# Kernel optimization log

Hardware: AMD Instinct MI355X
Metric: run time of the kernel (lower is better)

Reference implementation:

```python
import jax, jax.numpy as jnp
import numpy as np

WEIGHT_ENERGY = 0.1
WEIGHT_COV = 0.005
EPS = 1e-9
COV_EPS = 1e-6
TWO_PI = 2.0 * np.pi


def setup_inputs() -> dict:
    key = jax.random.key(0)
    k1, k2 = jax.random.split(key)
    z = jax.random.normal(k1, (16, 256, 64, 32), dtype=jnp.float32)
    gamma = jax.random.uniform(k2, (16, 256, 64, 8), dtype=jnp.float32)
    return {"z": z, "gamma": gamma}


def _gmm_loss(z, gamma):
    # z: [B,T,F,D], gamma: [B,T,F,K]
    D = z.shape[-1]
    N = z.shape[0] * z.shape[1] * z.shape[2]
    sum_gamma = jnp.sum(gamma, axis=(0, 1, 2))            # [K]
    phi = sum_gamma / N                                    # [K]
    mu = jnp.einsum('btfk,btfd->kd', gamma, z) / sum_gamma[:, None]  # [K,D]
    z_mu = z[..., None, :] - mu                            # [B,T,F,K,D]
    # covariance per component (gamma-weighted outer products)
    cov = jnp.einsum('btfk,btfkd,btfke->kde', gamma, z_mu, z_mu) / sum_gamma[:, None, None]
    eye = jnp.eye(D, dtype=z.dtype)
    cov = cov + CO_EPS_I(eye)
    cov_k = cov + EPS * eye                                # [K,D,D]
    cov_inv = jnp.linalg.inv(cov_k)                        # [K,D,D]
    L = jnp.linalg.cholesky(cov_k * TWO_PI)                # [K,D,D]
    det_cov = jnp.prod(jnp.diagonal(L, axis1=-2, axis2=-1), axis=-1)  # [K] (= sqrt(det(2pi*cov)))
    cov_diag = jnp.sum(1.0 / jnp.diagonal(cov_k, axis1=-2, axis2=-1))
    # quadratic-form energy, fused reduction over D
    E_z = -0.5 * jnp.einsum('btfkd,kde,btfke->btfk', z_mu, cov_inv, z_mu)
    E_z = jnp.exp(E_z)
    E_z = -jnp.log(jnp.sum(phi * E_z / jnp.sqrt(det_cov), axis=-1) + COV_EPS)
    sample_energy = jnp.mean(E_z)
    sample_energy = jnp.where(jnp.isfinite(sample_energy), sample_energy, 0.0)
    cov_diag = jnp.where(jnp.isfinite(cov_diag), cov_diag, 0.0)
    return WEIGHT_ENERGY * sample_energy + WEIGHT_COV * cov_diag


def CO_EPS_I(eye):
    return COV_EPS * eye


def reference(z, gamma):
    return _gmm_loss(z, gamma)
```

## Files before the change

kernel.cpp:

```cpp
#include <hip/hip_runtime.h>
#include <hip/hip_bf16.h>
#include <math.h>

#define NS (16*256*64)
#define NCHUNK (NS/64)
#define D 32
#define K 8

typedef __attribute__((ext_vector_type(8))) short bf16x8;
typedef __attribute__((ext_vector_type(8))) float f32x8;
typedef __attribute__((ext_vector_type(8))) __bf16 bf16v8;
typedef __attribute__((ext_vector_type(16))) float f32x16;

#define WS_ENERGY   0
#define WS_COVDIAG  1
#define WS_DONE     2
#define WS_C        16
#define WS_COEF     24
#define WS_SG       32
#define WS_S1       64
#define WS_S2       1024
#define WS_FRAGA    9216
#define WS_FRAGB    13312
#define WS_PART     16384
#define PART_STRIDE 8456

__device__ __forceinline__ bf16x8 cvt8(f32x8 v) {
    union { bf16v8 h; bf16x8 s; } u;
    u.h = __builtin_convertvector(v, bf16v8);
    return u.s;
}
__device__ __forceinline__ unsigned short f2bf1(float f) {
    union { __bf16 h; unsigned short s; } u;
    u.h = (__bf16)f;
    return u.s;
}
__device__ __forceinline__ float bf2f(unsigned short u) {
    union { unsigned u32; float f; } v;
    v.u32 = ((unsigned)u) << 16;
    return v.f;
}
__device__ __forceinline__ float rdlane(float v, int lane) {
    return __uint_as_float(__builtin_amdgcn_readlane(__float_as_uint(v), lane));
}

__global__ __launch_bounds__(256) void k_moments(const float* __restrict__ z,
                                                 const float* __restrict__ g,
                                                 float* __restrict__ part) {
    __shared__ __align__(16) unsigned short zbt[32][72];
    __shared__ __align__(16) unsigned short gbt[8][72];
    const int t   = threadIdx.x;
    const int w   = t >> 6;
    const int l   = t & 63;
    const int col = l & 31;
    const int nh  = l >> 5;
    const int k0  = 2 * w;
    const int sz  = t >> 2;
    const int dq  = (t & 3) * 8;

    f32x16 acc0 = {}, acc1 = {};
    float s1a = 0.f, s1b = 0.f, sga = 0.f, sgb = 0.f;

    int c = blockIdx.x;
    float4 za, zb4, ga4, gb4;
    {
        const float* zp = z + ((size_t)(c * 64 + sz)) * 32 + dq;
        za  = *(const float4*)zp;
        zb4 = *(const float4*)(zp + 4);
        if (t < 64) {
            const float* gp = g + ((size_t)(c * 64 + t)) * 8;
            ga4 = *(const float4*)gp;
            gb4 = *(const float4*)(gp + 4);
        }
    }

    for (; c < NCHUNK; c += gridDim.x) {
        __syncthreads();
        {
            float zf8[8] = {za.x, za.y, za.z, za.w, zb4.x, zb4.y, zb4.z, zb4.w};
#pragma unroll
            for (int i = 0; i < 8; i++) {
                int d = dq + i;
                zbt[d][sz ^ (((d >> 3) & 3) << 3)] = f2bf1(zf8[i]);
            }
            if (t < 64) {
                float gf8[8] = {ga4.x, ga4.y, ga4.z, ga4.w, gb4.x, gb4.y, gb4.z, gb4.w};
#pragma unroll
                for (int k = 0; k < 8; k++) gbt[k][t] = f2bf1(gf8[k]);
            }
        }
        {
            int cn = c + gridDim.x;
            if (cn < NCHUNK) {
                const float* zp = z + ((size_t)(cn * 64 + sz)) * 32 + dq;
                za  = *(const float4*)zp;
                zb4 = *(const float4*)(zp + 4);
                if (t < 64) {
                    const float* gp = g + ((size_t)(cn * 64 + t)) * 8;
                    ga4 = *(const float4*)gp;
                    gb4 = *(const float4*)(gp + 4);
                }
            }
        }
        __syncthreads();
        const int xs = ((col >> 3) & 3) << 3;
#pragma unroll
        for (int sc = 0; sc < 4; sc++) {
            const int s0 = sc * 16 + nh * 8;
            bf16x8 af = *(const bf16x8*)&zbt[col][s0 ^ xs];
            bf16x8 g0 = *(const bf16x8*)&gbt[k0][s0];
            bf16x8 g1 = *(const bf16x8*)&gbt[k0 + 1][s0];
            f32x8 p0, p1;
#pragma unroll
            for (int j = 0; j < 8; j++) {
                float zf = bf2f((unsigned short)af[j]);
                float ga = bf2f((unsigned short)g0[j]);
                float gb = bf2f((unsigned short)g1[j]);
                p0[j] = ga * zf;
                p1[j] = gb * zf;
                s1a += p0[j];  s1b += p1[j];
                sga += ga;     sgb += gb;
            }
            acc0 = __builtin_amdgcn_mfma_f32_32x32x16_bf16(af, cvt8(p0), acc0, 0, 0, 0);
            acc1 = __builtin_amdgcn_mfma_f32_32x32x16_bf16(af, cvt8(p1), acc1, 0, 0, 0);
        }
    }
    s1a += __shfl_xor(s1a, 32);  s1b += __shfl_xor(s1b, 32);
    sga += __shfl_xor(sga, 32);  sgb += __shfl_xor(sgb, 32);

    float* pb = part + (size_t)blockIdx.x * PART_STRIDE;
#pragma unroll
    for (int r = 0; r < 16; r++) {
        int row = (r & 3) + 8 * (r >> 2) + 4 * nh;
        pb[(size_t)k0 * 1024 + row * 32 + col]       = acc0[r];
        pb[(size_t)(k0 + 1) * 1024 + row * 32 + col] = acc1[r];
    }
    if (l < 32) {
        pb[8192 + k0 * 32 + col]       = s1a;
        pb[8192 + (k0 + 1) * 32 + col] = s1b;
    }
    if (l == 0) { pb[8448 + k0] = sga; pb[8448 + k0 + 1] = sgb; }
}

__global__ __launch_bounds__(1024) void k_reduce(float* __restrict__ ws, int nblk) {
    __shared__ float red[16][64];
    const int t  = threadIdx.x;
    const int el = t & 63;
    const int bg = t >> 6;
    const int e  = blockIdx.x * 64 + el;
    const float* part = ws + WS_PART;
    float s = 0.0f;
    if (e < PART_STRIDE) {
        for (int b = bg; b < nblk; b += 16)
            s += part[(size_t)b * PART_STRIDE + e];
    }
    red[bg][el] = s;
    __syncthreads();
#pragma unroll
    for (int h = 8; h > 0; h >>= 1) {
        if (bg < h) red[bg][el] += red[bg + h][el];
        __syncthreads();
    }
    if (bg == 0 && e < PART_STRIDE) {
        float v = red[0][el];
        if (e < 8192)       ws[WS_S2 + e] = v;
        else if (e < 8448)  ws[WS_S1 + (e - 8192)] = v;
        else                ws[WS_SG + (e - 8448)] = v;
    }
    if (blockIdx.x == 0) {
        if (t < 512) ws[WS_FRAGB + t] = 0.0f;
        if (t == 0) {
            ws[WS_ENERGY] = 0.0f;
            ws[WS_COVDIAG] = 0.0f;
            ((unsigned*)ws)[WS_DONE] = 0u;
        }
    }
}

__global__ __launch_bounds__(64) void k_prep(float* __restrict__ ws) {
    __shared__ float Am[32][33];
    __shared__ float mus[32];
    __shared__ float bLs[32];

    const int k   = blockIdx.x;
    const int l   = threadIdx.x;
    const int c32 = l & 31;
    const bool right = l >= 32;

    const float sgk = ws[WS_SG + k];
    if (l < 32) mus[l] = ws[WS_S1 + k * 32 + l] / sgk;
    __syncthreads();
    const float mc  = mus[c32];
    const float rsg = 1.0f / sgk;

    float x[32];
    float dval = 1.0f;
#pragma unroll
    for (int r = 0; r < 32; r++) {
        float v;
        if (right) {
            v = (r == c32) ? 1.0f : 0.0f;
        } else {
            v = ws[WS_S2 + k * 1024 + r * 32 + c32] * rsg - mus[r] * mc;
            if (r == c32) { v += 1.0e-6f + 1.0e-9f; dval = v; }
        }
        x[r] = v;
    }

    {
        float tdi = right ? 0.0f : 1.0f / dval;
#pragma unroll
        for (int m = 1; m < 64; m <<= 1) tdi += __shfl_xor(tdi, m);
        if (l == 0) atomicAdd(&ws[WS_COVDIAG], tdi);
    }

    float logdet = 0.0f;
#pragma unroll
    for (int j = 0; j < 32; j++) {
        float piv = rdlane(x[j], j);
        float rp  = 1.0f / piv;
        logdet += __logf(piv);
        x[j] *= rp;
#pragma unroll
        for (int r = 0; r < 32; r++) {
            if (r == j) continue;
            float m = rdlane(x[r], j);
            x[r] -= m * x[j];
        }
    }
    if (right) {
#pragma unroll
        for (int r = 0; r < 32; r++) Am[r][c32] = x[r];
    }
    __syncthreads();

    if (l == 0) {
        float phi = sgk / (float)NS;
        ws[WS_COEF + k] = phi * __expf(-(8.0f * 1.8378770664093453f + 0.25f * logdet));
    }

    if (l < 32) {
        float s = 0.0f;
#pragma unroll
        for (int c = 0; c < 32; c++) s += Am[c32][c] * mus[c];
        bLs[c32] = s;
    }
    __syncthreads();
    {
        float cm = (l < 32) ? mus[c32] * bLs[c32] : 0.0f;
#pragma unroll
        for (int m = 1; m < 64; m <<= 1) cm += __shfl_xor(cm, m);
        if (l == 0) ws[WS_C + k] = cm;
    }

    {
        const int ph = l >> 5;
#pragma unroll
        for (int h = 0; h < 2; h++) {
            int r = c32, cb = ph * 8 + 16 * h;
            unsigned uu[4];
#pragma unroll
            for (int q = 0; q < 4; q++) {
                unsigned lo2 = f2bf1(Am[r][cb + 2 * q]);
                unsigned hi2 = f2bf1(Am[r][cb + 2 * q + 1]);
                uu[q] = lo2 | (hi2 << 16);
            }
            ((uint4*)(ws + WS_FRAGA))[(k * 2 + h) * 64 + l] = make_uint4(uu[0], uu[1], uu[2], uu[3]);
        }
        if (c32 == k) {
#pragma unroll
            for (int h = 0; h < 2; h++) {
                int cb = ph * 8 + 16 * h;
                unsigned uu[4];
#pragma unroll
                for (int q = 0; q < 4; q++) {
                    unsigned lo2 = f2bf1(bLs[cb + 2 * q]);
                    unsigned hi2 = f2bf1(bLs[cb + 2 * q + 1]);
                    uu[q] = lo2 | (hi2 << 16);
                }
                ((uint4*)(ws + WS_FRAGB))[h * 64 + l] = make_uint4(uu[0], uu[1], uu[2], uu[3]);
            }
        }
    }
}

__global__ __launch_bounds__(512) void k_energy(const float* __restrict__ z,
                                                float* __restrict__ ws,
                                                float* __restrict__ out) {
    __shared__ float redw[8];
    const int t   = threadIdx.x;
    const int w   = t >> 6;
    const int l   = t & 63;
    const int col = l & 31;
    const int nh  = l >> 5;

    const uint4* fragA = (const uint4*)(ws + WS_FRAGA);
    const uint4* fragB = (const uint4*)(ws + WS_FRAGB);
    float cf[8], cc[8];
#pragma unroll
    for (int k = 0; k < 8; k++) { cf[k] = ws[WS_COEF + k]; cc[k] = ws[WS_C + k]; }
    uint4 fbu0 = fragB[l];
    uint4 fbu1 = fragB[64 + l];

    float En = 0.0f;
    for (int ci = 0; ci < 2; ci++) {
        const int chunk = (blockIdx.x * 8 + w) * 2 + ci;
        const int n0 = chunk * 32;
        const float* zb = z + (size_t)(n0 + col) * 32 + nh * 8;
        float4 a0 = *(const float4*)(zb + 0);
        float4 a1 = *(const float4*)(zb + 4);
        float4 a2 = *(const float4*)(zb + 16);
        float4 a3 = *(const float4*)(zb + 20);
        f32x8 zlo = {a0.x,a0.y,a0.z,a0.w,a1.x,a1.y,a1.z,a1.w};
        f32x8 zhi = {a2.x,a2.y,a2.z,a2.w,a3.x,a3.y,a3.z,a3.w};
        bf16x8 b0 = cvt8(zlo), b1 = cvt8(zhi);
        float olo[4], ohi[4];
#pragma unroll
        for (int j = 0; j < 4; j++) {
            float mlo = nh ? zlo[j] : zlo[j + 4];
            float mhi = nh ? zhi[j] : zhi[j + 4];
            olo[j] = __shfl_xor(mlo, 32);
            ohi[j] = __shfl_xor(mhi, 32);
        }
        float zdot[16];
#pragma unroll
        for (int j = 0; j < 4; j++) {
            zdot[j]      = nh ? olo[j]     : zlo[j];
            zdot[4 + j]  = nh ? zlo[4 + j] : olo[j];
            zdot[8 + j]  = nh ? ohi[j]     : zhi[j];
            zdot[12 + j] = nh ? zhi[4 + j] : ohi[j];
        }
        f32x16 acc2 = {};
        acc2 = __builtin_amdgcn_mfma_f32_32x32x16_bf16(*(const bf16x8*)&fbu0, b0, acc2, 0, 0, 0);
        acc2 = __builtin_amdgcn_mfma_f32_32x32x16_bf16(*(const bf16x8*)&fbu1, b1, acc2, 0, 0, 0);
        float oth[4];
#pragma unroll
        for (int r = 0; r < 4; r++) oth[r] = __shfl_xor(acc2[r], 32);
        float pk[8];
#pragma unroll
        for (int k = 0; k < 8; k++) {
            uint4 fa0u = fragA[(k * 2 + 0) * 64 + l];
            uint4 fa1u = fragA[(k * 2 + 1) * 64 + l];
            f32x16 acc = {};
            acc = __builtin_amdgcn_mfma_f32_32x32x16_bf16(*(const bf16x8*)&fa0u, b0, acc, 0, 0, 0);
            acc = __builtin_amdgcn_mfma_f32_32x32x16_bf16(*(const bf16x8*)&fa1u, b1, acc, 0, 0, 0);
            float p = 0.0f;
#pragma unroll
            for (int r = 0; r < 16; r++) p += acc[r] * zdot[r];
            p += __shfl_xor(p, 32);
            pk[k] = p;
        }
        float ssum = 0.0f;
#pragma unroll
        for (int k = 0; k < 8; k++) {
            float d2 = (k < 4) ? (nh ? oth[k] : acc2[k]) : (nh ? acc2[k - 4] : oth[k - 4]);
            float E = pk[k] - 2.0f * d2 + cc[k];
            ssum += cf[k] * __expf(-0.5f * E);
        }
        En += -__logf(ssum + 1.0e-6f);
    }
#pragma unroll
    for (int m = 1; m < 64; m <<= 1) En += __shfl_xor(En, m);
    if (l == 0) redw[w] = En;
    __syncthreads();
    if (t == 0) {
        float s = 0.0f;
#pragma unroll
        for (int i = 0; i < 8; i++) s += redw[i];
        atomicAdd(&ws[WS_ENERGY], s);
        __threadfence();
        unsigned old = atomicAdd((unsigned*)ws + WS_DONE, 1u);
        if (old == gridDim.x - 1) {
            float se = atomicAdd(&ws[WS_ENERGY], 0.0f);
            se = se * 0.5f / (float)NS;
            if (!isfinite(se)) se = 0.0f;
            float cd = ws[WS_COVDIAG];
            if (!isfinite(cd)) cd = 0.0f;
            out[0] = 0.1f * se + 0.005f * cd;
        }
    }
}

extern "C" void kernel_launch(void* const* d_in, const int* in_sizes, int n_in,
                              void* d_out, int out_size, void* d_ws, size_t ws_size,
                              hipStream_t stream) {
    const float* z = (const float*)d_in[0];
    const float* g = (const float*)d_in[1];
    float* out = (float*)d_out;
    float* ws  = (float*)d_ws;

    long avail = (long)(ws_size / 4) - WS_PART;
    int nblk = (int)(avail / PART_STRIDE);
    if (nblk > 512) nblk = 512;
    if (nblk < 1)   nblk = 1;

    k_moments<<<nblk, 256, 0, stream>>>(z, g, ws + WS_PART);
    k_reduce<<<(PART_STRIDE + 63) / 64, 1024, 0, stream>>>(ws, nblk);
    k_prep<<<8, 64, 0, stream>>>(ws);
    k_energy<<<512, 512, 0, stream>>>(z, ws, out);
}
```

Before: 79.48 us.

## Fuse partial reduction and covariance prep into one last-block kernel

Merges the partial-sum reduction and the per-component covariance inversion into one kernel. The last block to finish, detected with an atomic counter, inverts all 8 covariances, one wavefront per component. Workspace scalars are now zeroed at the start of the moments kernel, and the gamma sums move out of the MFMA inner loop into the load stage, summed in fp32 and reduced once per block. This removes one kernel launch and some per-iteration ALU work. The trade-off is a serialized tail in a single block, and the explicit zeroing of the B-fragment buffer is dropped.

```diff
diff --git a/kernel.cpp b/kernel.cpp
--- a/kernel.cpp
+++ b/kernel.cpp
@@ -15,6 +15,7 @@
 #define WS_ENERGY   0
 #define WS_COVDIAG  1
 #define WS_DONE     2
+#define WS_DONE2    3
 #define WS_C        16
 #define WS_COEF     24
 #define WS_SG       32
@@ -46,10 +47,11 @@
 
 __global__ __launch_bounds__(256) void k_moments(const float* __restrict__ z,
                                                  const float* __restrict__ g,
-                                                 float* __restrict__ part) {
+                                                 float* __restrict__ ws) {
     __shared__ __align__(16) unsigned short zbt[32][72];
     __shared__ __align__(16) unsigned short gbt[8][72];
     const int t   = threadIdx.x;
+    const int bid = blockIdx.x;
     const int w   = t >> 6;
     const int l   = t & 63;
     const int col = l & 31;
@@ -58,10 +60,15 @@
     const int sz  = t >> 2;
     const int dq  = (t & 3) * 8;
 
+    if (bid == 0 && t < 64) ws[t] = 0.0f;
+
     f32x16 acc0 = {}, acc1 = {};
-    float s1a = 0.f, s1b = 0.f, sga = 0.f, sgb = 0.f;
-
-    int c = blockIdx.x;
+    float s1a = 0.f, s1b = 0.f;
+    float sg8[8];
+#pragma unroll
+    for (int k = 0; k < 8; k++) sg8[k] = 0.0f;
+
+    int c = bid;
     float4 za, zb4, ga4, gb4;
     {
         const float* zp = z + ((size_t)(c * 64 + sz)) * 32 + dq;
@@ -73,7 +80,6 @@
             gb4 = *(const float4*)(gp + 4);
         }
     }
-
     for (; c < NCHUNK; c += gridDim.x) {
         __syncthreads();
         {
@@ -86,7 +92,10 @@
             if (t < 64) {
                 float gf8[8] = {ga4.x, ga4.y, ga4.z, ga4.w, gb4.x, gb4.y, gb4.z, gb4.w};
 #pragma unroll
-                for (int k = 0; k < 8; k++) gbt[k][t] = f2bf1(gf8[k]);
+                for (int k = 0; k < 8; k++) {
+                    gbt[k][t] = f2bf1(gf8[k]);
+                    sg8[k] += gf8[k];
+                }
             }
         }
         {
@@ -114,21 +123,17 @@
 #pragma unroll
             for (int j = 0; j < 8; j++) {
                 float zf = bf2f((unsigned short)af[j]);
-                float ga = bf2f((unsigned short)g0[j]);
-                float gb = bf2f((unsigned short)g1[j]);
-                p0[j] = ga * zf;
-                p1[j] = gb * zf;
+                p0[j] = bf2f((unsigned short)g0[j]) * zf;
+                p1[j] = bf2f((unsigned short)g1[j]) * zf;
                 s1a += p0[j];  s1b += p1[j];
-                sga += ga;     sgb += gb;
             }
             acc0 = __builtin_amdgcn_mfma_f32_32x32x16_bf16(af, cvt8(p0), acc0, 0, 0, 0);
             acc1 = __builtin_amdgcn_mfma_f32_32x32x16_bf16(af, cvt8(p1), acc1, 0, 0, 0);
         }
     }
     s1a += __shfl_xor(s1a, 32);  s1b += __shfl_xor(s1b, 32);
-    sga += __shfl_xor(sga, 32);  sgb += __shfl_xor(sgb, 32);
-
-    float* pb = part + (size_t)blockIdx.x * PART_STRIDE;
+
+    float* pb = ws + WS_PART + (size_t)bid * PART_STRIDE;
 #pragma unroll
     for (int r = 0; r < 16; r++) {
         int row = (r & 3) + 8 * (r >> 2) + 4 * nh;
@@ -139,11 +144,24 @@
         pb[8192 + k0 * 32 + col]       = s1a;
         pb[8192 + (k0 + 1) * 32 + col] = s1b;
     }
-    if (l == 0) { pb[8448 + k0] = sga; pb[8448 + k0 + 1] = sgb; }
-}
-
-__global__ __launch_bounds__(1024) void k_reduce(float* __restrict__ ws, int nblk) {
+    if (t < 64) {
+#pragma unroll
+        for (int k = 0; k < 8; k++) {
+            float v = sg8[k];
+#pragma unroll
+            for (int m = 1; m < 64; m <<= 1) v += __shfl_xor(v, m);
+            if (t == 0) pb[8448 + k] = v;
+        }
+    }
+}
+
+__global__ __launch_bounds__(1024) void k_redprep(float* __restrict__ ws, int nblk) {
     __shared__ float red[16][64];
+    __shared__ float Am8[8][32][33];
+    __shared__ float mus8[8][32];
+    __shared__ float bLs8[8][32];
+    __shared__ unsigned lastflag;
+
     const int t  = threadIdx.x;
     const int el = t & 63;
     const int bg = t >> 6;
@@ -167,115 +185,107 @@
         else if (e < 8448)  ws[WS_S1 + (e - 8192)] = v;
         else                ws[WS_SG + (e - 8448)] = v;
     }
-    if (blockIdx.x == 0) {
-        if (t < 512) ws[WS_FRAGB + t] = 0.0f;
-        if (t == 0) {
-            ws[WS_ENERGY] = 0.0f;
-            ws[WS_COVDIAG] = 0.0f;
-            ((unsigned*)ws)[WS_DONE] = 0u;
-        }
-    }
-}
-
-__global__ __launch_bounds__(64) void k_prep(float* __restrict__ ws) {
-    __shared__ float Am[32][33];
-    __shared__ float mus[32];
-    __shared__ float bLs[32];
-
-    const int k   = blockIdx.x;
-    const int l   = threadIdx.x;
+    __syncthreads();
+    if (t == 0) {
+        __threadfence();
+        unsigned old = atomicAdd((unsigned*)ws + WS_DONE2, 1u);
+        lastflag = (old == gridDim.x - 1) ? 1u : 0u;
+    }
+    __syncthreads();
+    if (!lastflag) return;
+
+    const int w8  = t >> 6;
+    const int l   = t & 63;
     const int c32 = l & 31;
-    const bool right = l >= 32;
-
-    const float sgk = ws[WS_SG + k];
-    if (l < 32) mus[l] = ws[WS_S1 + k * 32 + l] / sgk;
-    __syncthreads();
-    const float mc  = mus[c32];
-    const float rsg = 1.0f / sgk;
-
-    float x[32];
-    float dval = 1.0f;
-#pragma unroll
-    for (int r = 0; r < 32; r++) {
-        float v;
+    const bool pa    = (w8 < 8);
+    const bool right = pa && (l >= 32);
+
+    float sgk = 1.0f;
+    if (pa) sgk = ws[WS_SG + w8];
+    if (pa && l < 32) mus8[w8][l] = ws[WS_S1 + w8 * 32 + l] / sgk;
+    __syncthreads();
+
+    float logdet = 0.0f;
+    if (pa) {
+        const float mc  = mus8[w8][c32];
+        const float rsg = 1.0f / sgk;
+        float x[32];
+        float dval = 1.0f;
+#pragma unroll
+        for (int r = 0; r < 32; r++) {
+            float v;
+            if (right) {
+                v = (r == c32) ? 1.0f : 0.0f;
+            } else {
+                v = ws[WS_S2 + w8 * 1024 + r * 32 + c32] * rsg - mus8[w8][r] * mc;
+                if (r == c32) { v += 1.0e-6f + 1.0e-9f; dval = v; }
+            }
+            x[r] = v;
+        }
+        {
+            float tdi = right ? 0.0f : 1.0f / dval;
+#pragma unroll
+            for (int m = 1; m < 64; m <<= 1) tdi += __shfl_xor(tdi, m);
+            if (l == 0) atomicAdd(&ws[WS_COVDIAG], tdi);
+        }
+#pragma unroll
+        for (int j = 0; j < 32; j++) {
+            float piv = rdlane(x[j], j);
+            float rp  = 1.0f / piv;
+            logdet += __logf(piv);
+            x[j] *= rp;
+#pragma unroll
+            for (int r = 0; r < 32; r++) {
+                if (r == j) continue;
+                float m = rdlane(x[r], j);
+                x[r] -= m * x[j];
+            }
+        }
         if (right) {
-            v = (r == c32) ? 1.0f : 0.0f;
-        } else {
-            v = ws[WS_S2 + k * 1024 + r * 32 + c32] * rsg - mus[r] * mc;
-            if (r == c32) { v += 1.0e-6f + 1.0e-9f; dval = v; }
-        }
-        x[r] = v;
-    }
-
-    {
-        float tdi = right ? 0.0f : 1.0f / dval;
-#pragma unroll
-        for (int m = 1; m < 64; m <<= 1) tdi += __shfl_xor(tdi, m);
-        if (l == 0) atomicAdd(&ws[WS_COVDIAG], tdi);
-    }
-
-    float logdet = 0.0f;
-#pragma unroll
-    for (int j = 0; j < 32; j++) {
-        float piv = rdlane(x[j], j);
-        float rp  = 1.0f / piv;
-        logdet += __logf(piv);
-        x[j] *= rp;
-#pragma unroll
-        for (int r = 0; r < 32; r++) {
-            if (r == j) continue;
-            float m = rdlane(x[r], j);
-            x[r] -= m * x[j];
-        }
-    }
-    if (right) {
-#pragma unroll
-        for (int r = 0; r < 32; r++) Am[r][c32] = x[r];
-    }
-    __syncthreads();
-
-    if (l == 0) {
-        float phi = sgk / (float)NS;
-        ws[WS_COEF + k] = phi * __expf(-(8.0f * 1.8378770664093453f + 0.25f * logdet));
-    }
-
-    if (l < 32) {
-        float s = 0.0f;
-#pragma unroll
-        for (int c = 0; c < 32; c++) s += Am[c32][c] * mus[c];
-        bLs[c32] = s;
-    }
-    __syncthreads();
-    {
-        float cm = (l < 32) ? mus[c32] * bLs[c32] : 0.0f;
+#pragma unroll
+            for (int r = 0; r < 32; r++) Am8[w8][r][c32] = x[r];
+        }
+        if (l == 0) {
+            float phi = sgk / (float)NS;
+            ws[WS_COEF + w8] = phi * __expf(-(8.0f * 1.8378770664093453f + 0.25f * logdet));
+        }
+    }
+    __syncthreads();
+    if (pa && l < 32) {
+        float s2 = 0.0f;
+#pragma unroll
+        for (int c = 0; c < 32; c++) s2 += Am8[w8][c32][c] * mus8[w8][c];
+        bLs8[w8][c32] = s2;
+    }
+    __syncthreads();
+    if (pa) {
+        float cm = (l < 32) ? mus8[w8][c32] * bLs8[w8][c32] : 0.0f;
 #pragma unroll
         for (int m = 1; m < 64; m <<= 1) cm += __shfl_xor(cm, m);
-        if (l == 0) ws[WS_C + k] = cm;
-    }
-
-    {
+        if (l == 0) ws[WS_C + w8] = cm;
+
         const int ph = l >> 5;
 #pragma unroll
         for (int h = 0; h < 2; h++) {
-            int r = c32, cb = ph * 8 + 16 * h;
+            int cb = ph * 8 + 16 * h;
             unsigned uu[4];
 #pragma unroll
             for (int q = 0; q < 4; q++) {
-                unsigned lo2 = f2bf1(Am[r][cb + 2 * q]);
-                unsigned hi2 = f2bf1(Am[r][cb + 2 * q + 1]);
+                unsigned lo2 = f2bf1(Am8[w8][c32][cb + 2 * q]);
+                unsigned hi2 = f2bf1(Am8[w8][c32][cb + 2 * q + 1]);
                 uu[q] = lo2 | (hi2 << 16);
             }
-            ((uint4*)(ws + WS_FRAGA))[(k * 2 + h) * 64 + l] = make_uint4(uu[0], uu[1], uu[2], uu[3]);
-        }
-        if (c32 == k) {
+            ((uint4*)(ws + WS_FRAGA))[(w8 * 2 + h) * 64 + l] = make_uint4(uu[0], uu[1], uu[2], uu[3]);
+        }
+        if (c32 == w8) {
 #pragma unroll
             for (int h = 0; h < 2; h++) {
                 int cb = ph * 8 + 16 * h;
                 unsigned uu[4];
 #pragma unroll
                 for (int q = 0; q < 4; q++) {
-                    unsigned lo2 = f2bf1(bLs[cb + 2 * q]);
-                    unsigned hi2 = f2bf1(bLs[cb + 2 * q + 1]);
+                    unsigned lo2 = f2bf1(bLs8[w8][cb + 2 * q]);
+                    unsigned hi2 = f2bf1(bLs8[w8][cb + 2 * q + 1]);
                     uu[q] = lo2 | (hi2 << 16);
                 }
                 ((uint4*)(ws + WS_FRAGB))[h * 64 + l] = make_uint4(uu[0], uu[1], uu[2], uu[3]);
@@ -394,8 +404,7 @@
     if (nblk > 512) nblk = 512;
     if (nblk < 1)   nblk = 1;
 
-    k_moments<<<nblk, 256, 0, stream>>>(z, g, ws + WS_PART);
-    k_reduce<<<(PART_STRIDE + 63) / 64, 1024, 0, stream>>>(ws, nblk);
-    k_prep<<<8, 64, 0, stream>>>(ws);
+    k_moments<<<nblk, 256, 0, stream>>>(z, g, ws);
+    k_redprep<<<(PART_STRIDE + 63) / 64, 1024, 0, stream>>>(ws, nblk);
     k_energy<<<512, 512, 0, stream>>>(z, ws, out);
 }
```

Measured after the change: 82.10 us. 1.03x slower.
